# Performance work log

Measured on AMD Instinct MI355X. Metric: run time of the kernel, lower is better.

Reference implementation:

```python
import jax, jax.numpy as jnp
import numpy as np
from jax import lax

WIN_SIZE = 11
SIGMA = 1.5
CHANNELS = 3
C1 = (0.01 * 255) ** 2
C2 = (0.03 * 255) ** 2


def fspecial_gauss(size, sigma, channels):
    x, y = np.mgrid[-size // 2 + 1:size // 2 + 1, -size // 2 + 1:size // 2 + 1]
    g = np.exp(-((x ** 2 + y ** 2) / (2.0 * sigma ** 2)))
    g = (g / g.sum()).astype(np.float32)
    # depthwise kernel, OIHW with I=1, O=channels
    return jnp.asarray(np.tile(g[None, None], (channels, 1, 1, 1)))


def _gauss_filter(x, win):
    # depthwise valid conv, NCHW
    return lax.conv_general_dilated(
        x, win, window_strides=(1, 1), padding='VALID',
        feature_group_count=x.shape[1],
        dimension_numbers=('NCHW', 'OIHW', 'NCHW'))


def setup_inputs() -> dict:
    key = jax.random.key(0)
    k1, k2 = jax.random.split(key)
    X = jax.random.uniform(k1, (32, 3, 512, 512), dtype=jnp.float32)
    Y = jax.random.uniform(k2, (32, 3, 512, 512), dtype=jnp.float32)
    win = fspecial_gauss(WIN_SIZE, SIGMA, CHANNELS)
    return {"X": X, "Y": Y, "win": win}


def reference(X, Y, win):
    mu1 = _gauss_filter(X, win)
    mu2 = _gauss_filter(Y, win)
    mu1_sq = mu1 * mu1
    mu2_sq = mu2 * mu2
    mu1_mu2 = mu1 * mu2
    sigma1_sq = _gauss_filter(X * X, win) - mu1_sq
    sigma2_sq = _gauss_filter(Y * Y, win) - mu2_sq
    sigma12 = _gauss_filter(X * Y, win) - mu1_mu2
    cs_map = jax.nn.relu((2 * sigma12 + C2) / (sigma1_sq + sigma2_sq + C2))
    ssim_map = (2 * mu1_mu2 + C1) / (mu1_sq + mu2_sq + C1) * cs_map
    ssim_val = jnp.mean(ssim_map, axis=(1, 2, 3))  # per-image SSIM
    return 1.0 - jnp.mean(ssim_val)  # as_loss=True
```

## Files before the change

### kernel.cpp

```cpp
#include <hip/hip_runtime.h>
#include <math.h>


#define WIN   11
#define IMG   512
#define OUT_N 502
#define TO_R  32
#define TO_C  64
#define TI_C  (TO_C + WIN - 1)
#define VB_W  76
#define C1F   6.5025f
#define C2F   58.5225f

struct GaussW { float w[WIN]; };

__global__ __launch_bounds__(256) void ssim_v4_kernel(
    const float* __restrict__ X, const float* __restrict__ Y,
    GaussW gw, double* __restrict__ acc)
{
    __shared__ float vb[5][TO_R][VB_W];

    const int plane = blockIdx.z;
    const int ox0 = blockIdx.x * TO_C;
    const int oy0 = blockIdx.y * TO_R;
    const float* Xp = X + (size_t)plane * IMG * IMG;
    const float* Yp = Y + (size_t)plane * IMG * IMG;
    const int tid = threadIdx.x;

    for (int item = tid; item < 4 * TI_C; item += 256) {
        const int s = item / TI_C;
        const int c = item - s * TI_C;
        int gc = ox0 + c; if (gc > IMG - 1) gc = IMG - 1;
        const int r0 = oy0 + s * 8;

        float a0[8] = {0}, a1[8] = {0}, a2[8] = {0}, a3[8] = {0}, a4[8] = {0};
#pragma unroll
        for (int k = 0; k < 18; ++k) {
            int gr = r0 + k; if (gr > IMG - 1) gr = IMG - 1;
            size_t off = (size_t)gr * IMG + gc;
            float x = Xp[off];
            float y = Yp[off];
            float xx = x * x, yy = y * y, xy = x * y;
            const int jlo = (k > 10) ? (k - 10) : 0;
            const int jhi = (k < 7) ? k : 7;
#pragma unroll
            for (int j = jlo; j <= jhi; ++j) {
                float wv = gw.w[k - j];
                a0[j] += wv * x;
                a1[j] += wv * y;
                a2[j] += wv * xx;
                a3[j] += wv * yy;
                a4[j] += wv * xy;
            }
        }
#pragma unroll
        for (int j = 0; j < 8; ++j) {
            int i = s * 8 + j;
            vb[0][i][c] = a0[j];
            vb[1][i][c] = a1[j];
            vb[2][i][c] = a2[j];
            vb[3][i][c] = a3[j];
            vb[4][i][c] = a4[j];
        }
    }
    __syncthreads();

    const int t  = tid & 15;
    const int i0 = tid >> 4;
    const int c0 = 4 * t;
    float psum = 0.f;

#pragma unroll
    for (int pass = 0; pass < 2; ++pass) {
        const int i = i0 + 16 * pass;
        const int gi = oy0 + i;
        float m[5][4];
#pragma unroll
        for (int f = 0; f < 5; ++f) {
            float v[16];
            const float4* p = (const float4*)&vb[f][i][c0];
#pragma unroll
            for (int q = 0; q < 4; ++q) {
                float4 tt = p[q];
                v[4 * q + 0] = tt.x; v[4 * q + 1] = tt.y;
                v[4 * q + 2] = tt.z; v[4 * q + 3] = tt.w;
            }
#pragma unroll
            for (int oc = 0; oc < 4; ++oc) {
                float s = 0.f;
#pragma unroll
                for (int k = 0; k < WIN; ++k) s += gw.w[k] * v[oc + k];
                m[f][oc] = s;
            }
        }
#pragma unroll
        for (int oc = 0; oc < 4; ++oc) {
            int gj = ox0 + c0 + oc;
            if (gi < OUT_N && gj < OUT_N) {
                float m1 = m[0][oc], m2 = m[1][oc];
                float mu1s = m1 * m1, mu2s = m2 * m2, mu12 = m1 * m2;
                float sig1 = m[2][oc] - mu1s;
                float sig2 = m[3][oc] - mu2s;
                float sig12 = m[4][oc] - mu12;
                float cs = (2.f * sig12 + C2F) / (sig1 + sig2 + C2F);
                cs = fmaxf(cs, 0.f);
                psum += (2.f * mu12 + C1F) / (mu1s + mu2s + C1F) * cs;
            }
        }
    }

#pragma unroll
    for (int off = 32; off > 0; off >>= 1)
        psum += __shfl_down(psum, off, 64);
    __shared__ float wsum[4];
    if ((tid & 63) == 0) wsum[tid >> 6] = psum;
    __syncthreads();
    if (tid == 0) {
        float s = wsum[0] + wsum[1] + wsum[2] + wsum[3];
        atomicAdd(acc, (double)s);
    }
}

__global__ void ssim_finalize_kernel(const double* __restrict__ acc,
                                     float* __restrict__ out)
{
    if (threadIdx.x == 0 && blockIdx.x == 0) {
        const double count = (double)96 * OUT_N * OUT_N;
        out[0] = (float)(1.0 - (*acc) / count);
    }
}

extern "C" void kernel_launch(void* const* d_in, const int* in_sizes, int n_in,
                              void* d_out, int out_size, void* d_ws, size_t ws_size,
                              hipStream_t stream) {
    (void)in_sizes; (void)n_in; (void)out_size; (void)ws_size;
    const float* X = (const float*)d_in[0];
    const float* Y = (const float*)d_in[1];
    float* out = (float*)d_out;
    double* acc = (double*)d_ws;

    hipMemsetAsync(d_ws, 0, sizeof(double), stream);

    GaussW gw;
    {
        double g[WIN], s = 0.0;
        for (int i = 0; i < WIN; ++i) {
            double d = (double)(i - 5);
            g[i] = exp(-(d * d) / (2.0 * 1.5 * 1.5));
            s += g[i];
        }
        for (int i = 0; i < WIN; ++i) gw.w[i] = (float)(g[i] / s);
    }

    dim3 grid((OUT_N + TO_C - 1) / TO_C,
              (OUT_N + TO_R - 1) / TO_R,
              96);
    ssim_v4_kernel<<<grid, 256, 0, stream>>>(X, Y, gw, acc);
    ssim_finalize_kernel<<<1, 64, 0, stream>>>(acc, out);
}
```

Baseline: 316.4 us.

## Assign vertical strips per wave, widen horizontal outputs per thread, use fast reciprocal

Each wave now owns one 8-row strip of the vertical pass, with lanes looping over columns, so the vertical-pass divide and modulo are removed. The horizontal pass gives each thread 8 outputs from 18 loaded values in a single pass, down from 4 outputs over two passes, which cuts redundant shared-memory reads. The shared-memory pitch goes from 76 to 77 to ease bank conflicts, but this rules out float4 loads. The two SSIM divisions are merged into one num/den product computed with the hardware approximate reciprocal. That is slightly less accurate, and the relu is now applied to the numerator, which keeps the same sign logic only when both denominators are positive.

```diff
diff --git a/kernel.cpp b/kernel.cpp
--- a/kernel.cpp
+++ b/kernel.cpp
@@ -8,13 +8,13 @@
 #define TO_R  32
 #define TO_C  64
 #define TI_C  (TO_C + WIN - 1)
-#define VB_W  76
+#define VB_W  77
 #define C1F   6.5025f
 #define C2F   58.5225f
 
 struct GaussW { float w[WIN]; };
 
-__global__ __launch_bounds__(256) void ssim_v4_kernel(
+__global__ __launch_bounds__(256) void ssim_v5_kernel(
     const float* __restrict__ X, const float* __restrict__ Y,
     GaussW gw, double* __restrict__ acc)
 {
@@ -25,87 +25,81 @@
     const int oy0 = blockIdx.y * TO_R;
     const float* Xp = X + (size_t)plane * IMG * IMG;
     const float* Yp = Y + (size_t)plane * IMG * IMG;
-    const int tid = threadIdx.x;
+    const int tid  = threadIdx.x;
+    const int wave = tid >> 6;
+    const int lane = tid & 63;
 
-    for (int item = tid; item < 4 * TI_C; item += 256) {
-        const int s = item / TI_C;
-        const int c = item - s * TI_C;
-        int gc = ox0 + c; if (gc > IMG - 1) gc = IMG - 1;
+    {
+        const int s  = wave;
         const int r0 = oy0 + s * 8;
+        for (int c = lane; c < TI_C; c += 64) {
+            int gc = ox0 + c; if (gc > IMG - 1) gc = IMG - 1;
 
-        float a0[8] = {0}, a1[8] = {0}, a2[8] = {0}, a3[8] = {0}, a4[8] = {0};
+            float a0[8] = {0}, a1[8] = {0}, a2[8] = {0}, a3[8] = {0}, a4[8] = {0};
 #pragma unroll
-        for (int k = 0; k < 18; ++k) {
-            int gr = r0 + k; if (gr > IMG - 1) gr = IMG - 1;
-            size_t off = (size_t)gr * IMG + gc;
-            float x = Xp[off];
-            float y = Yp[off];
-            float xx = x * x, yy = y * y, xy = x * y;
-            const int jlo = (k > 10) ? (k - 10) : 0;
-            const int jhi = (k < 7) ? k : 7;
+            for (int k = 0; k < 18; ++k) {
+                int gr = r0 + k; if (gr > IMG - 1) gr = IMG - 1;
+                size_t off = (size_t)gr * IMG + gc;
+                float x = Xp[off];
+                float y = Yp[off];
+                float xx = x * x, yy = y * y, xy = x * y;
+                const int jlo = (k > 10) ? (k - 10) : 0;
+                const int jhi = (k < 7) ? k : 7;
 #pragma unroll
-            for (int j = jlo; j <= jhi; ++j) {
-                float wv = gw.w[k - j];
-                a0[j] += wv * x;
-                a1[j] += wv * y;
-                a2[j] += wv * xx;
-                a3[j] += wv * yy;
-                a4[j] += wv * xy;
+                for (int j = jlo; j <= jhi; ++j) {
+                    float wv = gw.w[k - j];
+                    a0[j] += wv * x;
+                    a1[j] += wv * y;
+                    a2[j] += wv * xx;
+                    a3[j] += wv * yy;
+                    a4[j] += wv * xy;
+                }
             }
-        }
 #pragma unroll
-        for (int j = 0; j < 8; ++j) {
-            int i = s * 8 + j;
-            vb[0][i][c] = a0[j];
-            vb[1][i][c] = a1[j];
-            vb[2][i][c] = a2[j];
-            vb[3][i][c] = a3[j];
-            vb[4][i][c] = a4[j];
+            for (int j = 0; j < 8; ++j) {
+                int i = s * 8 + j;
+                vb[0][i][c] = a0[j];
+                vb[1][i][c] = a1[j];
+                vb[2][i][c] = a2[j];
+                vb[3][i][c] = a3[j];
+                vb[4][i][c] = a4[j];
+            }
         }
     }
     __syncthreads();
 
-    const int t  = tid & 15;
-    const int i0 = tid >> 4;
-    const int c0 = 4 * t;
+    const int i  = tid >> 3;
+    const int c0 = (tid & 7) * 8;
+    const int gi = oy0 + i;
+    float m[5][8];
+#pragma unroll
+    for (int f = 0; f < 5; ++f) {
+        float v[18];
+#pragma unroll
+        for (int k = 0; k < 18; ++k) v[k] = vb[f][i][c0 + k];
+#pragma unroll
+        for (int oc = 0; oc < 8; ++oc) {
+            float s = 0.f;
+#pragma unroll
+            for (int k = 0; k < WIN; ++k) s += gw.w[k] * v[oc + k];
+            m[f][oc] = s;
+        }
+    }
+
     float psum = 0.f;
-
 #pragma unroll
-    for (int pass = 0; pass < 2; ++pass) {
-        const int i = i0 + 16 * pass;
-        const int gi = oy0 + i;
-        float m[5][4];
-#pragma unroll
-        for (int f = 0; f < 5; ++f) {
-            float v[16];
-            const float4* p = (const float4*)&vb[f][i][c0];
-#pragma unroll
-            for (int q = 0; q < 4; ++q) {
-                float4 tt = p[q];
-                v[4 * q + 0] = tt.x; v[4 * q + 1] = tt.y;
-                v[4 * q + 2] = tt.z; v[4 * q + 3] = tt.w;
-            }
-#pragma unroll
-            for (int oc = 0; oc < 4; ++oc) {
-                float s = 0.f;
-#pragma unroll
-                for (int k = 0; k < WIN; ++k) s += gw.w[k] * v[oc + k];
-                m[f][oc] = s;
-            }
-        }
-#pragma unroll
-        for (int oc = 0; oc < 4; ++oc) {
-            int gj = ox0 + c0 + oc;
-            if (gi < OUT_N && gj < OUT_N) {
-                float m1 = m[0][oc], m2 = m[1][oc];
-                float mu1s = m1 * m1, mu2s = m2 * m2, mu12 = m1 * m2;
-                float sig1 = m[2][oc] - mu1s;
-                float sig2 = m[3][oc] - mu2s;
-                float sig12 = m[4][oc] - mu12;
-                float cs = (2.f * sig12 + C2F) / (sig1 + sig2 + C2F);
-                cs = fmaxf(cs, 0.f);
-                psum += (2.f * mu12 + C1F) / (mu1s + mu2s + C1F) * cs;
-            }
+    for (int oc = 0; oc < 8; ++oc) {
+        int gj = ox0 + c0 + oc;
+        if (gi < OUT_N && gj < OUT_N) {
+            float m1 = m[0][oc], m2 = m[1][oc];
+            float mu1s = m1 * m1, mu2s = m2 * m2, mu12 = m1 * m2;
+            float sig1  = m[2][oc] - mu1s;
+            float sig2  = m[3][oc] - mu2s;
+            float sig12 = m[4][oc] - mu12;
+            float num = (2.f * mu12 + C1F) * (2.f * sig12 + C2F);
+            float den = (mu1s + mu2s + C1F) * (sig1 + sig2 + C2F);
+            num = fmaxf(num, 0.f);
+            psum += num * __builtin_amdgcn_rcpf(den);
         }
     }
 
@@ -155,6 +149,6 @@
     dim3 grid((OUT_N + TO_C - 1) / TO_C,
               (OUT_N + TO_R - 1) / TO_R,
               96);
-    ssim_v4_kernel<<<grid, 256, 0, stream>>>(X, Y, gw, acc);
+    ssim_v5_kernel<<<grid, 256, 0, stream>>>(X, Y, gw, acc);
     ssim_finalize_kernel<<<1, 64, 0, stream>>>(acc, out);
 }
```

After: 313.8 us. About the same (-0.8%).
